# Optimization experiments

Measured on AMD Instinct MI355X. Metric: run time of the kernel, lower is better.

Reference implementation:

```python
import jax, jax.numpy as jnp
import numpy as np

N_OBJ, N_REG = 4096, 8192
D_HO = D_HR = 512
GATE_W = 128
E = 131072


def setup_inputs() -> dict:
    key = jax.random.key(0)
    ks = jax.random.split(key, 10)
    s = 1.0 / np.sqrt(D_HO + D_HR)
    return {
        "feature_obj": jax.random.normal(ks[0], (N_OBJ, D_HO), jnp.float32),
        "feature_region": jax.random.normal(ks[1], (N_REG, D_HR), jnp.float32),
        # edge lists (tgt, src) equivalent to np.where(select_mat > 0)
        "r2o_tgt": jnp.sort(jax.random.randint(ks[2], (E,), 0, N_OBJ, jnp.int32)),
        "r2o_src": jax.random.randint(ks[3], (E,), 0, N_REG, jnp.int32),
        "o2r_tgt": jnp.sort(jax.random.randint(ks[4], (E,), 0, N_REG, jnp.int32)),
        "o2r_src": jax.random.randint(ks[5], (E,), 0, N_OBJ, jnp.int32),
        # attention gate Linear(dim_src+dim_tgt -> gate_width), bias=True
        "gw_r2o": jax.random.uniform(ks[6], (GATE_W, D_HR + D_HO), jnp.float32, -s, s),
        "gb_r2o": jnp.zeros((GATE_W,), jnp.float32),
        "gw_o2r": jax.random.uniform(ks[7], (GATE_W, D_HO + D_HR), jnp.float32, -s, s),
        "gb_o2r": jnp.zeros((GATE_W,), jnp.float32),
        # transform Sequential(ReLU, Linear(dim -> dim, bias=True))
        "tw_r2o": jax.random.uniform(ks[8], (D_HO, D_HR), jnp.float32, -s, s),
        "tb_r2o": jnp.zeros((D_HO,), jnp.float32),
        "tw_o2r": jax.random.uniform(ks[9], (D_HR, D_HO), jnp.float32, -s, s),
        "tb_o2r": jnp.zeros((D_HR,), jnp.float32),
    }


def _message(tgt_feat, src_feat, tgt_idx, src_idx, gw, gb, num_tgt):
    # gather per-edge source/target features: [E, ds], [E, dt]
    src = src_feat[src_idx]
    tgt = tgt_feat[tgt_idx]
    # Attention_Module: gate = mean(sigmoid(W @ relu(cat(src, tgt)) + b))
    g = jax.nn.relu(jnp.concatenate([src, tgt], axis=-1))
    gate = jnp.mean(jax.nn.sigmoid(g @ gw.T + gb), axis=-1, keepdims=True)  # [E, 1]
    msg = src * gate
    agg = jax.ops.segment_sum(msg, tgt_idx, num_segments=num_tgt)
    # mps_use_average=True -> per-target mean; targets with no edges stay zero
    cnt = jax.ops.segment_sum(jnp.ones((tgt_idx.shape[0], 1), msg.dtype), tgt_idx, num_segments=num_tgt)
    return agg / jnp.maximum(cnt, 1.0)


def reference(feature_obj, feature_region, r2o_tgt, r2o_src, o2r_tgt, o2r_src,
              gw_r2o, gb_r2o, gw_o2r, gb_o2r, tw_r2o, tb_r2o, tw_o2r, tb_o2r):
    m_r2o = _message(feature_obj, feature_region, r2o_tgt, r2o_src, gw_r2o, gb_r2o, N_OBJ)
    out_obj = feature_obj + jax.nn.relu(m_r2o) @ tw_r2o.T + tb_r2o
    m_o2r = _message(feature_region, feature_obj, o2r_tgt, o2r_src, gw_o2r, gb_o2r, N_REG)
    out_reg = feature_region + jax.nn.relu(m_o2r) @ tw_o2r.T + tb_o2r
    return (out_obj, out_reg)
```

## Files before the change

### kernel.cpp

```cpp
#include <hip/hip_runtime.h>

constexpr int N_OBJ = 4096, N_REG = 8192, D = 512, GW = 128, NE = 131072;

typedef __attribute__((ext_vector_type(8))) short short8;
typedef __attribute__((ext_vector_type(4))) float f32x4;

__device__ inline short f2bf(float f) {
  unsigned u = __builtin_bit_cast(unsigned, f);
  unsigned r = (u + 0x7FFF + ((u >> 16) & 1)) >> 16;
  return (short)r;
}
__device__ inline float bf2f(short s) {
  return __builtin_bit_cast(float, (unsigned)(((unsigned short)s) << 16));
}

__global__ void csr_all(const int* __restrict__ t_r2o, const int* __restrict__ t_o2r,
                        int* __restrict__ off_r2o, int* __restrict__ off_o2r) {
  int i = blockIdx.x * blockDim.x + threadIdx.x;
  const int* tgt; int* off; int t;
  if (i <= N_OBJ) { tgt = t_r2o; off = off_r2o; t = i; }
  else {
    i -= N_OBJ + 1;
    if (i > N_REG) return;
    tgt = t_o2r; off = off_o2r; t = i;
  }
  int lo = 0, hi = NE;
  while (lo < hi) {
    int mid = (lo + hi) >> 1;
    if (tgt[mid] < t) lo = mid + 1; else hi = mid;
  }
  off[t] = lo;
}

__global__ __launch_bounds__(256) void cast_all(
    const float* __restrict__ feat_reg, const float* __restrict__ feat_obj,
    const float* __restrict__ gw_r2o, const float* __restrict__ gw_o2r,
    const float* __restrict__ tw_r2o, const float* __restrict__ tw_o2r,
    short* __restrict__ raw_reg, short* __restrict__ relu_reg,
    short* __restrict__ raw_obj, short* __restrict__ relu_obj,
    short* __restrict__ Wreg, short* __restrict__ Wobj,
    short* __restrict__ btw_r2o, short* __restrict__ btw_o2r) {
  int i = blockIdx.x * 256 + threadIdx.x;
  if (i < 1572864) {
    const float* src; short* draw; short* drelu; int j = i;
    if (j < 1048576) { src = feat_reg; draw = raw_reg; drelu = relu_reg; }
    else { j -= 1048576; src = feat_obj; draw = raw_obj; drelu = relu_obj; }
    float4 v = ((const float4*)src)[j];
    ((short4*)draw)[j] = make_short4(f2bf(v.x), f2bf(v.y), f2bf(v.z), f2bf(v.w));
    ((short4*)drelu)[j] = make_short4(f2bf(fmaxf(v.x, 0.f)), f2bf(fmaxf(v.y, 0.f)),
                                      f2bf(fmaxf(v.z, 0.f)), f2bf(fmaxf(v.w, 0.f)));
    return;
  }
  i -= 1572864;
  const float* src; short* dst; int di;
  if (i < 32768) {
    int row = i >> 7, c4 = i & 127;
    src = (row < 128) ? gw_r2o + (size_t)row * 1024 + c4 * 4
                      : gw_o2r + (size_t)(row - 128) * 1024 + 512 + c4 * 4;
    dst = Wreg; di = i;
  } else if (i < 65536) {
    int k = i - 32768, row = k >> 7, c4 = k & 127;
    src = (row < 128) ? gw_r2o + (size_t)row * 1024 + 512 + c4 * 4
                      : gw_o2r + (size_t)(row - 128) * 1024 + c4 * 4;
    dst = Wobj; di = k;
  } else if (i < 131072) { di = i - 65536; src = tw_r2o + (size_t)di * 4; dst = btw_r2o; }
  else                   { di = i - 131072; src = tw_o2r + (size_t)di * 4; dst = btw_o2r; }
  float4 v = *(const float4*)src;
  ((short4*)dst)[di] = make_short4(f2bf(v.x), f2bf(v.y), f2bf(v.z), f2bf(v.w));
}

struct GemmPair {
  const short* A[2]; const short* B[2];
  const float* res[2]; const float* bias[2];
  void* C[2];
  int nb0;
  int nxb;
  int ldc;
};

template<bool EPI>
__global__ __launch_bounds__(256) void gemm_pair(GemmPair gp) {
  __shared__ short As[128 * 32];
  __shared__ short Bs[128 * 32];
  int b = blockIdx.x;
  const int pi = (b >= gp.nb0) ? 1 : 0;
  if (pi) b -= gp.nb0;
  const int bx = b % gp.nxb, by = b / gp.nxb;
  const short* __restrict__ A = gp.A[pi];
  const short* __restrict__ B = gp.B[pi];
  const int ldc = gp.ldc;
  const int tid = threadIdx.x;
  const int lane = tid & 63, w = tid >> 6;
  const int m0 = by * 128, n0 = bx * 128;
  const int wm = (w >> 1) * 64, wn = (w & 1) * 64;
  const int sr = lane >> 2, sc = (lane & 3) * 8;
  const int fr = lane & 15, fk = (lane >> 4) * 8;

  f32x4 acc[4][4];
#pragma unroll
  for (int i = 0; i < 4; ++i)
#pragma unroll
    for (int j = 0; j < 4; ++j) acc[i][j] = (f32x4){0.f, 0.f, 0.f, 0.f};

  for (int k0 = 0; k0 < 512; k0 += 32) {
#pragma unroll
    for (int h = 0; h < 2; ++h) {
      int rg = w * 32 + h * 16;
      const short* ga = A + (size_t)(m0 + rg + sr) * 512 + k0 + sc;
      const short* gb = B + (size_t)(n0 + rg + sr) * 512 + k0 + sc;
      __builtin_amdgcn_global_load_lds(
          (const __attribute__((address_space(1))) void*)ga,
          (__attribute__((address_space(3))) void*)&As[rg * 32], 16, 0, 0);
      __builtin_amdgcn_global_load_lds(
          (const __attribute__((address_space(1))) void*)gb,
          (__attribute__((address_space(3))) void*)&Bs[rg * 32], 16, 0, 0);
    }
    __syncthreads();
    short8 a[4], bfr[4];
#pragma unroll
    for (int i = 0; i < 4; ++i)
      a[i] = *(const short8*)&As[(wm + i * 16 + fr) * 32 + fk];
#pragma unroll
    for (int j = 0; j < 4; ++j)
      bfr[j] = *(const short8*)&Bs[(wn + j * 16 + fr) * 32 + fk];
#pragma unroll
    for (int i = 0; i < 4; ++i)
#pragma unroll
      for (int j = 0; j < 4; ++j)
        acc[i][j] = __builtin_amdgcn_mfma_f32_16x16x32_bf16(a[i], bfr[j], acc[i][j], 0, 0, 0);
    __syncthreads();
  }

  if (EPI) {
    float* C = (float*)gp.C[pi];
    const float* res = gp.res[pi];
    const float* bias = gp.bias[pi];
#pragma unroll
    for (int i = 0; i < 4; ++i)
#pragma unroll
      for (int j = 0; j < 4; ++j) {
        int n = n0 + wn + j * 16 + fr;
#pragma unroll
        for (int r = 0; r < 4; ++r) {
          int m = m0 + wm + i * 16 + (lane >> 4) * 4 + r;
          C[(size_t)m * ldc + n] = acc[i][j][r] + res[(size_t)m * ldc + n] + bias[n];
        }
      }
  } else {
    short* C = (short*)gp.C[pi];
#pragma unroll
    for (int i = 0; i < 4; ++i)
#pragma unroll
      for (int j = 0; j < 4; ++j) {
        int n = n0 + wn + j * 16 + fr;
#pragma unroll
        for (int r = 0; r < 4; ++r) {
          int m = m0 + wm + i * 16 + (lane >> 4) * 4 + r;
          C[(size_t)m * ldc + n] = f2bf(acc[i][j][r]);
        }
      }
  }
}

__global__ __launch_bounds__(256) void gate2(
    const short* __restrict__ Preg, const short* __restrict__ Pobj,
    const int* __restrict__ r2o_tgt, const int* __restrict__ r2o_src,
    const int* __restrict__ o2r_tgt, const int* __restrict__ o2r_src,
    const float* __restrict__ gb_r2o, const float* __restrict__ gb_o2r,
    float* __restrict__ gate_r2o, float* __restrict__ gate_o2r) {
  const int tid = threadIdx.x, lane = tid & 31;
  const int e = blockIdx.x * 8 + (tid >> 5);
  const short* pa; const short* pb; const float* gbp; float* out;
  if (blockIdx.y == 0) {
    pa = Preg + (size_t)r2o_src[e] * 256 + lane * 4;
    pb = Pobj + (size_t)r2o_tgt[e] * 256 + lane * 4;
    gbp = gb_r2o; out = gate_r2o;
  } else {
    pa = Pobj + (size_t)o2r_src[e] * 256 + 128 + lane * 4;
    pb = Preg + (size_t)o2r_tgt[e] * 256 + 128 + lane * 4;
    gbp = gb_o2r; out = gate_o2r;
  }
  short4 a4 = *(const short4*)pa;
  short4 b4 = *(const short4*)pb;
  float4 bb = *(const float4*)&gbp[lane * 4];
  float sum = 1.f / (1.f + __expf(-(bf2f(a4.x) + bf2f(b4.x) + bb.x)))
            + 1.f / (1.f + __expf(-(bf2f(a4.y) + bf2f(b4.y) + bb.y)))
            + 1.f / (1.f + __expf(-(bf2f(a4.z) + bf2f(b4.z) + bb.z)))
            + 1.f / (1.f + __expf(-(bf2f(a4.w) + bf2f(b4.w) + bb.w)));
#pragma unroll
  for (int msk = 16; msk >= 1; msk >>= 1) sum += __shfl_xor(sum, msk, 64);
  if (lane == 0) out[e] = sum * (1.0f / GW);
}

__global__ __launch_bounds__(256) void segsum2(
    const short* __restrict__ raw_reg, const short* __restrict__ raw_obj,
    const float* __restrict__ gate_r2o, const float* __restrict__ gate_o2r,
    const int* __restrict__ r2o_src, const int* __restrict__ o2r_src,
    const int* __restrict__ off_r2o, const int* __restrict__ off_o2r,
    short* __restrict__ m_obj, short* __restrict__ m_reg) {
  int t = blockIdx.x;
  const short* ftab; const float* gate; const int* src; const int* off; short* mo;
  if (t < N_OBJ) { ftab = raw_reg; gate = gate_r2o; src = r2o_src; off = off_r2o; mo = m_obj; }
  else { t -= N_OBJ; ftab = raw_obj; gate = gate_o2r; src = o2r_src; off = off_o2r; mo = m_reg; }
  const int e0 = off[t], e1 = off[t + 1];
  const int tid = threadIdx.x;
  float a0 = 0.f, a1 = 0.f;
  for (int e = e0; e < e1; ++e) {
    float g = gate[e];
    int s = src[e];
    short2 v = *(const short2*)(ftab + (size_t)s * D + tid * 2);
    a0 += bf2f(v.x) * g;
    a1 += bf2f(v.y) * g;
  }
  float inv = 1.0f / fmaxf((float)(e1 - e0), 1.0f);
  short2 o;
  o.x = f2bf(fmaxf(a0 * inv, 0.f));
  o.y = f2bf(fmaxf(a1 * inv, 0.f));
  *(short2*)(mo + (size_t)t * D + tid * 2) = o;
}

extern "C" void kernel_launch(void* const* d_in, const int* in_sizes, int n_in,
                              void* d_out, int out_size, void* d_ws, size_t ws_size,
                              hipStream_t stream) {
  const float* feat_obj = (const float*)d_in[0];
  const float* feat_reg = (const float*)d_in[1];
  const int*   r2o_tgt  = (const int*)d_in[2];
  const int*   r2o_src  = (const int*)d_in[3];
  const int*   o2r_tgt  = (const int*)d_in[4];
  const int*   o2r_src  = (const int*)d_in[5];
  const float* gw_r2o   = (const float*)d_in[6];
  const float* gb_r2o   = (const float*)d_in[7];
  const float* gw_o2r   = (const float*)d_in[8];
  const float* gb_o2r   = (const float*)d_in[9];
  const float* tw_r2o   = (const float*)d_in[10];
  const float* tb_r2o   = (const float*)d_in[11];
  const float* tw_o2r   = (const float*)d_in[12];
  const float* tb_o2r   = (const float*)d_in[13];
  float* out_obj = (float*)d_out;
  float* out_reg = out_obj + (size_t)N_OBJ * D;

  size_t cur = 0;
  auto alloc = [&](size_t bytes) -> void* {
    cur = (cur + 255) & ~(size_t)255;
    void* p = (char*)d_ws + cur;
    cur += bytes;
    return p;
  };
  int*   off_r2o = (int*)alloc((N_OBJ + 1) * sizeof(int));
  int*   off_o2r = (int*)alloc((N_REG + 1) * sizeof(int));
  short* raw_reg = (short*)alloc((size_t)N_REG * D * 2);
  short* relu_reg= (short*)alloc((size_t)N_REG * D * 2);
  short* raw_obj = (short*)alloc((size_t)N_OBJ * D * 2);
  short* relu_obj= (short*)alloc((size_t)N_OBJ * D * 2);
  short* Wreg    = (short*)alloc((size_t)256 * D * 2);
  short* Wobj    = (short*)alloc((size_t)256 * D * 2);
  short* btw_r2o = (short*)alloc((size_t)D * D * 2);
  short* btw_o2r = (short*)alloc((size_t)D * D * 2);
  short* Preg    = (short*)alloc((size_t)N_REG * 256 * 2);
  short* Pobj    = (short*)alloc((size_t)N_OBJ * 256 * 2);
  float* gate_r2o= (float*)alloc((size_t)NE * 4);
  float* gate_o2r= (float*)alloc((size_t)NE * 4);
  short* m_obj   = (short*)alloc((size_t)N_OBJ * D * 2);
  short* m_reg   = (short*)alloc((size_t)N_REG * D * 2);

  csr_all<<<49, 256, 0, stream>>>(r2o_tgt, o2r_tgt, off_r2o, off_o2r);
  cast_all<<<6912, 256, 0, stream>>>(feat_reg, feat_obj, gw_r2o, gw_o2r, tw_r2o, tw_o2r,
                                     raw_reg, relu_reg, raw_obj, relu_obj,
                                     Wreg, Wobj, btw_r2o, btw_o2r);

  GemmPair proj;
  proj.A[0] = relu_reg; proj.B[0] = Wreg; proj.C[0] = Preg;
  proj.A[1] = relu_obj; proj.B[1] = Wobj; proj.C[1] = Pobj;
  proj.res[0] = proj.res[1] = nullptr; proj.bias[0] = proj.bias[1] = nullptr;
  proj.nb0 = 2 * (N_REG / 128); proj.nxb = 2; proj.ldc = 256;
  gemm_pair<false><<<192, 256, 0, stream>>>(proj);

  gate2<<<dim3(NE / 8, 2), 256, 0, stream>>>(Preg, Pobj, r2o_tgt, r2o_src, o2r_tgt, o2r_src,
                                             gb_r2o, gb_o2r, gate_r2o, gate_o2r);

  segsum2<<<N_OBJ + N_REG, 256, 0, stream>>>(raw_reg, raw_obj, gate_r2o, gate_o2r,
                                             r2o_src, o2r_src, off_r2o, off_o2r,
                                             m_obj, m_reg);

  GemmPair tr;
  tr.A[0] = m_reg; tr.B[0] = btw_o2r; tr.res[0] = feat_reg; tr.bias[0] = tb_o2r; tr.C[0] = out_reg;
  tr.A[1] = m_obj; tr.B[1] = btw_r2o; tr.res[1] = feat_obj; tr.bias[1] = tb_r2o; tr.C[1] = out_obj;
  tr.nb0 = 4 * (N_REG / 128); tr.nxb = 4; tr.ldc = D;
  gemm_pair<true><<<384, 256, 0, stream>>>(tr);
}
```

Baseline: 232.0 us.

## Fuse per-edge gate computation into segment-sum kernel and merge CSR build into cast

The separate gate kernel, which wrote per-edge gate values to global memory, is folded into the segmented-sum kernel. Each target block now computes the gate on the fly, using the target projection loaded once per block and the source projection per edge. Edges are split across four wavefronts and combined through shared memory. The CSR offset binary search moves into the cast kernel to drop one launch. This removes the gate buffer round trip and a launch, at the cost of a cross-lane reduction per edge inside the aggregation loop.

```diff
diff --git a/kernel.cpp b/kernel.cpp
--- a/kernel.cpp
+++ b/kernel.cpp
@@ -14,33 +14,34 @@
   return __builtin_bit_cast(float, (unsigned)(((unsigned short)s) << 16));
 }
 
-__global__ void csr_all(const int* __restrict__ t_r2o, const int* __restrict__ t_o2r,
-                        int* __restrict__ off_r2o, int* __restrict__ off_o2r) {
-  int i = blockIdx.x * blockDim.x + threadIdx.x;
-  const int* tgt; int* off; int t;
-  if (i <= N_OBJ) { tgt = t_r2o; off = off_r2o; t = i; }
-  else {
-    i -= N_OBJ + 1;
-    if (i > N_REG) return;
-    tgt = t_o2r; off = off_o2r; t = i;
-  }
-  int lo = 0, hi = NE;
-  while (lo < hi) {
-    int mid = (lo + hi) >> 1;
-    if (tgt[mid] < t) lo = mid + 1; else hi = mid;
-  }
-  off[t] = lo;
-}
-
-__global__ __launch_bounds__(256) void cast_all(
+__global__ __launch_bounds__(256) void cast_csr(
     const float* __restrict__ feat_reg, const float* __restrict__ feat_obj,
     const float* __restrict__ gw_r2o, const float* __restrict__ gw_o2r,
     const float* __restrict__ tw_r2o, const float* __restrict__ tw_o2r,
+    const int* __restrict__ t_r2o, const int* __restrict__ t_o2r,
     short* __restrict__ raw_reg, short* __restrict__ relu_reg,
     short* __restrict__ raw_obj, short* __restrict__ relu_obj,
     short* __restrict__ Wreg, short* __restrict__ Wobj,
-    short* __restrict__ btw_r2o, short* __restrict__ btw_o2r) {
+    short* __restrict__ btw_r2o, short* __restrict__ btw_o2r,
+    int* __restrict__ off_r2o, int* __restrict__ off_o2r) {
   int i = blockIdx.x * 256 + threadIdx.x;
+  if (i >= 1769472) {
+    i -= 1769472;
+    const int* tgt; int* off; int t;
+    if (i <= N_OBJ) { tgt = t_r2o; off = off_r2o; t = i; }
+    else {
+      i -= N_OBJ + 1;
+      if (i > N_REG) return;
+      tgt = t_o2r; off = off_o2r; t = i;
+    }
+    int lo = 0, hi = NE;
+    while (lo < hi) {
+      int mid = (lo + hi) >> 1;
+      if (tgt[mid] < t) lo = mid + 1; else hi = mid;
+    }
+    off[t] = lo;
+    return;
+  }
   if (i < 1572864) {
     const float* src; short* draw; short* drelu; int j = i;
     if (j < 1048576) { src = feat_reg; draw = raw_reg; drelu = relu_reg; }
@@ -162,61 +163,54 @@
   }
 }
 
-__global__ __launch_bounds__(256) void gate2(
+__global__ __launch_bounds__(256) void fused_msg(
     const short* __restrict__ Preg, const short* __restrict__ Pobj,
-    const int* __restrict__ r2o_tgt, const int* __restrict__ r2o_src,
-    const int* __restrict__ o2r_tgt, const int* __restrict__ o2r_src,
-    const float* __restrict__ gb_r2o, const float* __restrict__ gb_o2r,
-    float* __restrict__ gate_r2o, float* __restrict__ gate_o2r) {
-  const int tid = threadIdx.x, lane = tid & 31;
-  const int e = blockIdx.x * 8 + (tid >> 5);
-  const short* pa; const short* pb; const float* gbp; float* out;
-  if (blockIdx.y == 0) {
-    pa = Preg + (size_t)r2o_src[e] * 256 + lane * 4;
-    pb = Pobj + (size_t)r2o_tgt[e] * 256 + lane * 4;
-    gbp = gb_r2o; out = gate_r2o;
-  } else {
-    pa = Pobj + (size_t)o2r_src[e] * 256 + 128 + lane * 4;
-    pb = Preg + (size_t)o2r_tgt[e] * 256 + 128 + lane * 4;
-    gbp = gb_o2r; out = gate_o2r;
-  }
-  short4 a4 = *(const short4*)pa;
-  short4 b4 = *(const short4*)pb;
-  float4 bb = *(const float4*)&gbp[lane * 4];
-  float sum = 1.f / (1.f + __expf(-(bf2f(a4.x) + bf2f(b4.x) + bb.x)))
-            + 1.f / (1.f + __expf(-(bf2f(a4.y) + bf2f(b4.y) + bb.y)))
-            + 1.f / (1.f + __expf(-(bf2f(a4.z) + bf2f(b4.z) + bb.z)))
-            + 1.f / (1.f + __expf(-(bf2f(a4.w) + bf2f(b4.w) + bb.w)));
-#pragma unroll
-  for (int msk = 16; msk >= 1; msk >>= 1) sum += __shfl_xor(sum, msk, 64);
-  if (lane == 0) out[e] = sum * (1.0f / GW);
-}
-
-__global__ __launch_bounds__(256) void segsum2(
     const short* __restrict__ raw_reg, const short* __restrict__ raw_obj,
-    const float* __restrict__ gate_r2o, const float* __restrict__ gate_o2r,
     const int* __restrict__ r2o_src, const int* __restrict__ o2r_src,
     const int* __restrict__ off_r2o, const int* __restrict__ off_o2r,
+    const float* __restrict__ gb_r2o, const float* __restrict__ gb_o2r,
     short* __restrict__ m_obj, short* __restrict__ m_reg) {
+  __shared__ float red[4][512];
   int t = blockIdx.x;
-  const short* ftab; const float* gate; const int* src; const int* off; short* mo;
-  if (t < N_OBJ) { ftab = raw_reg; gate = gate_r2o; src = r2o_src; off = off_r2o; mo = m_obj; }
-  else { t -= N_OBJ; ftab = raw_obj; gate = gate_o2r; src = o2r_src; off = off_o2r; mo = m_reg; }
+  const short* PA; const short* PB; const short* feat; const int* src;
+  const int* off; const float* gb; short* mo; int po;
+  if (t < N_OBJ) {
+    PA = Preg; PB = Pobj; feat = raw_reg; src = r2o_src; off = off_r2o;
+    gb = gb_r2o; mo = m_obj; po = 0;
+  } else {
+    t -= N_OBJ;
+    PA = Pobj; PB = Preg; feat = raw_obj; src = o2r_src; off = off_o2r;
+    gb = gb_o2r; mo = m_reg; po = 128;
+  }
+  const int tid = threadIdx.x, lane = tid & 63, w = tid >> 6;
   const int e0 = off[t], e1 = off[t + 1];
-  const int tid = threadIdx.x;
-  float a0 = 0.f, a1 = 0.f;
-  for (int e = e0; e < e1; ++e) {
-    float g = gate[e];
+  short2 pb2 = *(const short2*)&PB[(size_t)t * 256 + po + lane * 2];
+  float2 gb2 = *(const float2*)&gb[lane * 2];
+  const float c0 = bf2f(pb2.x) + gb2.x, c1 = bf2f(pb2.y) + gb2.y;
+  float acc[8] = {};
+  for (int e = e0 + w; e < e1; e += 4) {
     int s = src[e];
-    short2 v = *(const short2*)(ftab + (size_t)s * D + tid * 2);
-    a0 += bf2f(v.x) * g;
-    a1 += bf2f(v.y) * g;
-  }
-  float inv = 1.0f / fmaxf((float)(e1 - e0), 1.0f);
+    short2 pa2 = *(const short2*)&PA[(size_t)s * 256 + po + lane * 2];
+    short8 v = *(const short8*)&feat[(size_t)s * 512 + lane * 8];
+    float gs = 1.f / (1.f + __expf(-(bf2f(pa2.x) + c0)))
+             + 1.f / (1.f + __expf(-(bf2f(pa2.y) + c1)));
+#pragma unroll
+    for (int msk = 32; msk >= 1; msk >>= 1) gs += __shfl_xor(gs, msk, 64);
+    gs *= (1.0f / 128.0f);
+#pragma unroll
+    for (int j = 0; j < 8; ++j) acc[j] += bf2f(v[j]) * gs;
+  }
+  *(float4*)&red[w][lane * 8]     = (float4){acc[0], acc[1], acc[2], acc[3]};
+  *(float4*)&red[w][lane * 8 + 4] = (float4){acc[4], acc[5], acc[6], acc[7]};
+  __syncthreads();
+  const float inv = 1.0f / fmaxf((float)(e1 - e0), 1.0f);
+  const int d = tid * 2;
+  float s0 = red[0][d] + red[1][d] + red[2][d] + red[3][d];
+  float s1 = red[0][d + 1] + red[1][d + 1] + red[2][d + 1] + red[3][d + 1];
   short2 o;
-  o.x = f2bf(fmaxf(a0 * inv, 0.f));
-  o.y = f2bf(fmaxf(a1 * inv, 0.f));
-  *(short2*)(mo + (size_t)t * D + tid * 2) = o;
+  o.x = f2bf(fmaxf(s0 * inv, 0.f));
+  o.y = f2bf(fmaxf(s1 * inv, 0.f));
+  *(short2*)(mo + (size_t)t * 512 + d) = o;
 }
 
 extern "C" void kernel_launch(void* const* d_in, const int* in_sizes, int n_in,
@@ -258,15 +252,13 @@
   short* btw_o2r = (short*)alloc((size_t)D * D * 2);
   short* Preg    = (short*)alloc((size_t)N_REG * 256 * 2);
   short* Pobj    = (short*)alloc((size_t)N_OBJ * 256 * 2);
-  float* gate_r2o= (float*)alloc((size_t)NE * 4);
-  float* gate_o2r= (float*)alloc((size_t)NE * 4);
   short* m_obj   = (short*)alloc((size_t)N_OBJ * D * 2);
   short* m_reg   = (short*)alloc((size_t)N_REG * D * 2);
 
-  csr_all<<<49, 256, 0, stream>>>(r2o_tgt, o2r_tgt, off_r2o, off_o2r);
-  cast_all<<<6912, 256, 0, stream>>>(feat_reg, feat_obj, gw_r2o, gw_o2r, tw_r2o, tw_o2r,
+  cast_csr<<<6961, 256, 0, stream>>>(feat_reg, feat_obj, gw_r2o, gw_o2r, tw_r2o, tw_o2r,
+                                     r2o_tgt, o2r_tgt,
                                      raw_reg, relu_reg, raw_obj, relu_obj,
-                                     Wreg, Wobj, btw_r2o, btw_o2r);
+                                     Wreg, Wobj, btw_r2o, btw_o2r, off_r2o, off_o2r);
 
   GemmPair proj;
   proj.A[0] = relu_reg; proj.B[0] = Wreg; proj.C[0] = Preg;
@@ -275,12 +267,9 @@
   proj.nb0 = 2 * (N_REG / 128); proj.nxb = 2; proj.ldc = 256;
   gemm_pair<false><<<192, 256, 0, stream>>>(proj);
 
-  gate2<<<dim3(NE / 8, 2), 256, 0, stream>>>(Preg, Pobj, r2o_tgt, r2o_src, o2r_tgt, o2r_src,
-                                             gb_r2o, gb_o2r, gate_r2o, gate_o2r);
-
-  segsum2<<<N_OBJ + N_REG, 256, 0, stream>>>(raw_reg, raw_obj, gate_r2o, gate_o2r,
-                                             r2o_src, o2r_src, off_r2o, off_o2r,
-                                             m_obj, m_reg);
+  fused_msg<<<N_OBJ + N_REG, 256, 0, stream>>>(Preg, Pobj, raw_reg, raw_obj,
+                                               r2o_src, o2r_src, off_r2o, off_o2r,
+                                               gb_r2o, gb_o2r, m_obj, m_reg);
 
   GemmPair tr;
   tr.A[0] = m_reg; tr.B[0] = btw_o2r; tr.res[0] = feat_reg; tr.bias[0] = tb_o2r; tr.C[0] = out_reg;
```

New measurement: 197.7 us. 1.17x faster.
